# Kernel optimization log

Hardware: AMD Instinct MI355X
Metric: run time of the kernel (lower is better)

The kernel has to match this reference:

```python
import jax, jax.numpy as jnp
import numpy as np

CLASS_COUNT = 21
THRESHOLD = 0.5
ALPHA = 0.25
GAMMA = 2.0
VARIANCE = (0.1, 0.2)

B, A, N_OBJ = 32, 24576, 16


def point_form(boxes):
    # center form (cx, cy, w, h) -> point form (xmin, ymin, xmax, ymax)
    return jnp.concatenate([boxes[:, :2] - boxes[:, 2:] / 2,
                            boxes[:, :2] + boxes[:, 2:] / 2], axis=1)


def jaccard(truths, priors):
    # truths [N,4], priors [A,4] both in point form -> IoU [N, A]
    lt = jnp.maximum(truths[:, None, :2], priors[None, :, :2])
    rb = jnp.minimum(truths[:, None, 2:], priors[None, :, 2:])
    wh = jnp.clip(rb - lt, 0.0, None)
    inter = wh[..., 0] * wh[..., 1]
    area_t = ((truths[:, 2] - truths[:, 0]) * (truths[:, 3] - truths[:, 1]))[:, None]
    area_p = ((priors[:, 2] - priors[:, 0]) * (priors[:, 3] - priors[:, 1]))[None, :]
    return inter / (area_t + area_p - inter)


def match_one(labels, truths, anchors):
    # labels [N] int, truths [N,4] point form, anchors [A,4] center form
    overlaps = jaccard(truths, point_form(anchors))           # [N, A]
    best_prior_idx = jnp.argmax(overlaps, axis=1)             # [N]
    best_truth_overlap = jnp.max(overlaps, axis=0)            # [A]
    best_truth_idx = jnp.argmax(overlaps, axis=0)             # [A]
    # ensure every gt matches its best prior
    best_truth_overlap = best_truth_overlap.at[best_prior_idx].set(2.0)
    best_truth_idx = best_truth_idx.at[best_prior_idx].set(jnp.arange(truths.shape[0]))
    matches = truths[best_truth_idx]                          # [A, 4]
    conf = jnp.where(best_truth_overlap < THRESHOLD, 0, labels[best_truth_idx])
    # encode with variances
    g_cxcy = ((matches[:, :2] + matches[:, 2:]) * 0.5 - anchors[:, :2]) / (VARIANCE[0] * anchors[:, 2:])
    g_wh = jnp.log((matches[:, 2:] - matches[:, :2]) / anchors[:, 2:]) / VARIANCE[1]
    return conf, jnp.concatenate([g_cxcy, g_wh], axis=1)


def setup_inputs() -> dict:
    key = jax.random.key(0)
    k1, k2, k3, k4, k5, k6, k7 = jax.random.split(key, 7)
    class_preds = jax.random.normal(k1, (B, A, CLASS_COUNT), dtype=jnp.float32)
    loc_preds = jax.random.normal(k2, (B, A, 4), dtype=jnp.float32)
    # ground-truth boxes: random valid point-form boxes in [0,1]
    ctr = jax.random.uniform(k3, (B, N_OBJ, 2), minval=0.2, maxval=0.8)
    wh = jax.random.uniform(k4, (B, N_OBJ, 2), minval=0.05, maxval=0.3)
    loc_targets = jnp.clip(jnp.concatenate([ctr - wh / 2, ctr + wh / 2], axis=-1), 0.0, 1.0)
    class_targets = jax.random.randint(k5, (B, N_OBJ), 1, CLASS_COUNT)
    # anchors in center form
    a_ctr = jax.random.uniform(k6, (A, 2), minval=0.05, maxval=0.95)
    a_wh = jax.random.uniform(k7, (A, 2), minval=0.05, maxval=0.4)
    anchors = jnp.concatenate([a_ctr, a_wh], axis=1)
    return {"class_preds": class_preds, "loc_preds": loc_preds,
            "loc_targets": loc_targets, "anchors": anchors,
            "class_targets": class_targets}


def reference(class_preds, loc_preds, loc_targets, anchors, class_targets):
    conf, loc_t = jax.vmap(match_one, in_axes=(0, 0, None))(class_targets, loc_targets, anchors)
    pos = conf > 0                                            # [B, A]
    num_matched = jnp.sum(pos).astype(jnp.float32)
    # smooth L1 over positive anchors (sum reduction, beta=1)
    d = loc_preds - loc_t
    ad = jnp.abs(d)
    sl1 = jnp.where(ad < 1.0, 0.5 * d * d, ad - 0.5)
    loc_loss = jnp.sum(sl1 * pos[..., None].astype(sl1.dtype))
    # focal loss (drop background column 0)
    cp = class_preds.reshape(-1, CLASS_COUNT)[:, 1:]          # [B*A, C-1]
    t = jax.nn.one_hot(conf.reshape(-1), CLASS_COUNT, dtype=cp.dtype)[:, 1:]
    p = jax.nn.sigmoid(cp)
    pt = jnp.where(t > 0, p, 1.0 - p)
    w = (1.0 - pt) ** GAMMA
    w = jnp.where(t > 0, ALPHA * w, (1.0 - ALPHA) * w)
    # stable binary cross entropy with logits, weighted, sum reduction
    bce = jnp.maximum(cp, 0.0) - cp * t + jnp.log1p(jnp.exp(-jnp.abs(cp)))
    class_loss = jnp.sum(w * bce)
    class_loss = class_loss / num_matched
    loc_loss = loc_loss / num_matched
    return jnp.stack([class_loss, loc_loss, class_loss + loc_loss])
```

## Files before the change

kernel.cpp:

```cpp
#include <hip/hip_runtime.h>

#define A_COUNT 24576
#define B_COUNT 32
#define NOBJ 16
#define C_COUNT 21

#define NM 48
#define CHUNK (A_COUNT / NM)
#define NBLK_M (NM * B_COUNT)
#define NBLK_F 2048
#define GRID (NBLK_F + NBLK_M)
#define TOTAL4 (B_COUNT * A_COUNT * C_COUNT / 4)
#define STRIDE4F (NBLK_F * 256)

#define WS_BPP 0
#define WS_LOCP 196608
#define WS_CORP 202752
#define WS_POSP 208896
#define WS_CLSP 215040
#define WS_DLOC 223232
#define WS_DCLS 223360
#define WS_DPOS 223488

__device__ __forceinline__ unsigned long long pack_key(float iou, int a) {
    unsigned int ib = __float_as_uint(iou);
    return ((unsigned long long)ib << 32) | (unsigned long long)(0xFFFFFFFFu - (unsigned int)a);
}

__device__ __forceinline__ float iou_pf(float tx0, float ty0, float tx1, float ty1, float at,
                                        float x0, float y0, float x1, float y1, float ap) {
    float lx = fmaxf(tx0, x0), ly = fmaxf(ty0, y0);
    float rx = fminf(tx1, x1), ry = fminf(ty1, y1);
    float w = fmaxf(rx - lx, 0.0f), h = fmaxf(ry - ly, 0.0f);
    float inter = w * h;
    return inter * __builtin_amdgcn_rcpf(at + ap - inter);
}

__device__ __forceinline__ float sl1(float d) {
    float ad = fabsf(d);
    return (ad < 1.0f) ? 0.5f * d * d : ad - 0.5f;
}

__device__ __forceinline__ float loc_term(float4 t, float4 an, float4 lp) {
    float gx = ((t.x + t.z) * 0.5f - an.x) / (0.1f * an.z);
    float gy = ((t.y + t.w) * 0.5f - an.y) / (0.1f * an.w);
    float gw = __logf((t.z - t.x) / an.z) * 5.0f;
    float gh = __logf((t.w - t.y) / an.w) * 5.0f;
    return sl1(lp.x - gx) + sl1(lp.y - gy) + sl1(lp.z - gw) + sl1(lp.w - gh);
}

__device__ __forceinline__ float corr_term(float x) {
    float E = __expf(x);
    float den = 1.0f + E;
    float s = __builtin_amdgcn_rcpf(den);
    float p = E * s;
    float L = __logf(den);
    return 0.25f * s * s * (L - x) - 0.75f * p * p * L;
}

#define FOC(xval, rr, acc) {                                 \
    float E_ = __expf(xval);                                 \
    float den_ = 1.0f + E_;                                  \
    float s_ = __builtin_amdgcn_rcpf(den_);                  \
    float p_ = E_ * s_;                                      \
    float L_ = __logf(den_);                                 \
    float v_ = ((rr) == 0 || (rr) == 21) ? 0.0f : p_ * p_ * L_; \
    acc += v_; }

__global__ __launch_bounds__(256, 8) void k_phase1(const float* __restrict__ cls,
                                                   const float4* __restrict__ locp,
                                                   const float4* __restrict__ anchors,
                                                   const float4* __restrict__ truths,
                                                   const int* __restrict__ labels,
                                                   unsigned long long* __restrict__ bp_partial,
                                                   float* __restrict__ loc_partial,
                                                   float* __restrict__ corr_partial,
                                                   unsigned int* __restrict__ pos_partial,
                                                   float* __restrict__ cls_partial) {
    const int bid = blockIdx.x;
    const int tid = threadIdx.x;
    const int wv = tid >> 6, ln = tid & 63;
    __shared__ float s_red[4];

    if (bid < NBLK_F) {
        const float4* cls4 = (const float4*)cls;
        float acc0 = 0.0f, acc1 = 0.0f, acc2 = 0.0f, acc3 = 0.0f;
        int i = bid * 256 + tid;
        unsigned int f = (unsigned int)i * 4u;
        unsigned int dq = f / 21u;
        int r = (int)(f - dq * 21u);
        for (; i < TOTAL4; i += STRIDE4F) {
            float4 x4 = cls4[i];
            FOC(x4.x, r + 0, acc0); FOC(x4.y, r + 1, acc1);
            FOC(x4.z, r + 2, acc2); FOC(x4.w, r + 3, acc3);
            r += 8; if (r >= 21) r -= 21;
        }
        float cls_acc = 0.75f * ((acc0 + acc1) + (acc2 + acc3));
#pragma unroll
        for (int s = 32; s >= 1; s >>= 1) cls_acc += __shfl_xor(cls_acc, s);
        if (ln == 0) s_red[wv] = cls_acc;
        __syncthreads();
        if (tid == 0) cls_partial[bid] = s_red[0] + s_red[1] + s_red[2] + s_red[3];
        return;
    }

    const int mb = bid - NBLK_F;
    const int ch = mb % NM;
    const int b = mb / NM;
    __shared__ float4 s_t[NOBJ];
    __shared__ float s_area[NOBJ];
    __shared__ int s_lab[NOBJ];
    __shared__ unsigned long long s_w[NOBJ][4];
    if (tid < NOBJ) {
        float4 t = truths[b * NOBJ + tid];
        s_t[tid] = t;
        s_area[tid] = (t.z - t.x) * (t.w - t.y);
        s_lab[tid] = labels[b * NOBJ + tid];
    }
    __syncthreads();
    const int a0 = ch * CHUNK + tid;
    const int a1 = a0 + 256;
    float4 an0 = anchors[a0];
    float4 an1 = anchors[a1];
    float p0x0 = an0.x - an0.z * 0.5f, p0y0 = an0.y - an0.w * 0.5f;
    float p0x1 = an0.x + an0.z * 0.5f, p0y1 = an0.y + an0.w * 0.5f;
    float ap0 = (p0x1 - p0x0) * (p0y1 - p0y0);
    float p1x0 = an1.x - an1.z * 0.5f, p1y0 = an1.y - an1.w * 0.5f;
    float p1x1 = an1.x + an1.z * 0.5f, p1y1 = an1.y + an1.w * 0.5f;
    float ap1 = (p1x1 - p1x0) * (p1y1 - p1y0);
    float best0 = -1.0f, best1 = -1.0f;
    int idx0 = 0, idx1 = 0;
#pragma unroll
    for (int n = 0; n < NOBJ; ++n) {
        float4 t = s_t[n];
        float at = s_area[n];
        float iou0 = iou_pf(t.x, t.y, t.z, t.w, at, p0x0, p0y0, p0x1, p0y1, ap0);
        float iou1 = iou_pf(t.x, t.y, t.z, t.w, at, p1x0, p1y0, p1x1, p1y1, ap1);
        if (iou0 > best0) { best0 = iou0; idx0 = n; }
        if (iou1 > best1) { best1 = iou1; idx1 = n; }
        float lm = fmaxf(iou0, iou1);
        float m = lm;
#pragma unroll
        for (int s = 32; s >= 1; s >>= 1) m = fmaxf(m, __shfl_xor(m, s));
        unsigned long long mask = __ballot(lm == m);
        if (ln == __builtin_ctzll(mask)) {
            s_w[n][wv] = (iou0 == m) ? pack_key(iou0, a0) : pack_key(iou1, a1);
        }
    }
    __syncthreads();
    if (tid < NOBJ) {
        unsigned long long k = s_w[tid][0];
#pragma unroll
        for (int i = 1; i < 4; ++i) k = (s_w[tid][i] > k) ? s_w[tid][i] : k;
        bp_partial[(b * NOBJ + tid) * NM + ch] = k;
    }
    float loc_l = 0.0f, corr_acc = 0.0f;
    unsigned int pos = 0;
    if (!(best0 < 0.5f)) {
        pos++;
        loc_l += loc_term(s_t[idx0], an0, locp[(size_t)b * A_COUNT + a0]);
        corr_acc += corr_term(cls[((size_t)b * A_COUNT + a0) * C_COUNT + s_lab[idx0]]);
    }
    if (!(best1 < 0.5f)) {
        pos++;
        loc_l += loc_term(s_t[idx1], an1, locp[(size_t)b * A_COUNT + a1]);
        corr_acc += corr_term(cls[((size_t)b * A_COUNT + a1) * C_COUNT + s_lab[idx1]]);
    }
#pragma unroll
    for (int s = 32; s >= 1; s >>= 1) {
        loc_l += __shfl_xor(loc_l, s);
        corr_acc += __shfl_xor(corr_acc, s);
        pos += __shfl_xor(pos, s);
    }
    __shared__ float s_cr[4];
    __shared__ unsigned int s_pp[4];
    if (ln == 0) {
        s_red[wv] = loc_l;
        s_cr[wv] = corr_acc;
        s_pp[wv] = pos;
    }
    __syncthreads();
    if (tid == 0) {
        loc_partial[mb] = s_red[0] + s_red[1] + s_red[2] + s_red[3];
        corr_partial[mb] = s_cr[0] + s_cr[1] + s_cr[2] + s_cr[3];
        pos_partial[mb] = s_pp[0] + s_pp[1] + s_pp[2] + s_pp[3];
    }
}

__global__ __launch_bounds__(256) void k_fix(const float* __restrict__ cls,
                                             const float4* __restrict__ locp,
                                             const float4* __restrict__ anchors,
                                             const float4* __restrict__ truths,
                                             const int* __restrict__ labels,
                                             const unsigned long long* __restrict__ bp_partial,
                                             float* __restrict__ dloc,
                                             float* __restrict__ dcls,
                                             int* __restrict__ dpos) {
    const int b = blockIdx.x;
    const int tid = threadIdx.x;
    __shared__ int s_bp[NOBJ];
    {
        const int g = tid >> 4, l = tid & 15;
        const unsigned long long* pp = &bp_partial[(size_t)(b * NOBJ + g) * NM];
        unsigned long long k = pp[l];
#pragma unroll
        for (int kk = 1; kk < 3; ++kk) {
            unsigned long long v = pp[l + 16 * kk];
            k = (v > k) ? v : k;
        }
#pragma unroll
        for (int s = 8; s >= 1; s >>= 1) {
            unsigned long long o = __shfl_xor(k, s);
            k = (o > k) ? o : k;
        }
        if (l == 0) {
            unsigned int ia = 0xFFFFFFFFu - (unsigned int)(k & 0xFFFFFFFFull);
            s_bp[g] = (ia >= A_COUNT) ? -1 : (int)ia;
        }
    }
    __syncthreads();
    float d_loc = 0.0f, d_cls = 0.0f;
    int d_pos = 0;
    if (tid < NOBJ) {
        const int n = tid;
        const int q = s_bp[n];
        bool winner = (q >= 0);
        for (int n2 = n + 1; n2 < NOBJ; ++n2)
            if (s_bp[n2] == q) winner = false;
        if (winner) {
            float4 an = anchors[q];
            float px0 = an.x - an.z * 0.5f, py0 = an.y - an.w * 0.5f;
            float px1 = an.x + an.z * 0.5f, py1 = an.y + an.w * 0.5f;
            float ap = (px1 - px0) * (py1 - py0);
            float best = -1.0f;
            int idx = 0;
            for (int n2 = 0; n2 < NOBJ; ++n2) {
                float4 t = truths[b * NOBJ + n2];
                float at = (t.z - t.x) * (t.w - t.y);
                float iou = iou_pf(t.x, t.y, t.z, t.w, at, px0, py0, px1, py1, ap);
                if (iou > best) { best = iou; idx = n2; }
            }
            float4 lp = locp[(size_t)b * A_COUNT + q];
            if (!(best < 0.5f)) {
                d_pos -= 1;
                d_loc -= loc_term(truths[b * NOBJ + idx], an, lp);
                d_cls -= corr_term(cls[((size_t)b * A_COUNT + q) * C_COUNT + labels[b * NOBJ + idx]]);
            }
            d_pos += 1;
            d_loc += loc_term(truths[b * NOBJ + n], an, lp);
            d_cls += corr_term(cls[((size_t)b * A_COUNT + q) * C_COUNT + labels[b * NOBJ + n]]);
        }
    }
    if (tid < 64) {
#pragma unroll
        for (int s = 8; s >= 1; s >>= 1) {
            d_loc += __shfl_xor(d_loc, s);
            d_cls += __shfl_xor(d_cls, s);
            d_pos += __shfl_xor(d_pos, s);
        }
        if (tid == 0) {
            dloc[b] = d_loc;
            dcls[b] = d_cls;
            dpos[b] = d_pos;
        }
    }
}

__global__ __launch_bounds__(256) void k_final(const float* __restrict__ loc_partial,
                                               const float* __restrict__ corr_partial,
                                               const unsigned int* __restrict__ pos_partial,
                                               const float* __restrict__ cls_partial,
                                               const float* __restrict__ dloc,
                                               const float* __restrict__ dcls,
                                               const int* __restrict__ dpos,
                                               float* __restrict__ out) {
    const int tid = threadIdx.x;
    double loc = 0.0, clsv = 0.0;
    int pos = 0;
    for (int i = tid; i < NBLK_M; i += 256) {
        loc += (double)loc_partial[i];
        clsv += (double)corr_partial[i];
        pos += (int)pos_partial[i];
    }
    for (int i = tid; i < NBLK_F; i += 256) clsv += (double)cls_partial[i];
    if (tid < B_COUNT) {
        loc += (double)dloc[tid];
        clsv += (double)dcls[tid];
        pos += dpos[tid];
    }
#pragma unroll
    for (int s = 32; s >= 1; s >>= 1) {
        loc += __shfl_xor(loc, s);
        clsv += __shfl_xor(clsv, s);
        pos += __shfl_xor(pos, s);
    }
    __shared__ double s_l[4], s_c[4];
    __shared__ int s_p[4];
    if ((tid & 63) == 0) {
        s_l[tid >> 6] = loc;
        s_c[tid >> 6] = clsv;
        s_p[tid >> 6] = pos;
    }
    __syncthreads();
    if (tid == 0) {
        double L = s_l[0] + s_l[1] + s_l[2] + s_l[3];
        double Cv = s_c[0] + s_c[1] + s_c[2] + s_c[3];
        float nm = (float)(s_p[0] + s_p[1] + s_p[2] + s_p[3]);
        float cf = (float)Cv / nm;
        float lf = (float)L / nm;
        out[0] = cf;
        out[1] = lf;
        out[2] = cf + lf;
    }
}

extern "C" void kernel_launch(void* const* d_in, const int* in_sizes, int n_in,
                              void* d_out, int out_size, void* d_ws, size_t ws_size,
                              hipStream_t stream) {
    const float* cls = (const float*)d_in[0];
    const float4* locp = (const float4*)d_in[1];
    const float4* truths = (const float4*)d_in[2];
    const float4* anchors = (const float4*)d_in[3];
    const int* labels = (const int*)d_in[4];

    char* ws = (char*)d_ws;
    unsigned long long* bp_partial = (unsigned long long*)(ws + WS_BPP);
    float* loc_partial = (float*)(ws + WS_LOCP);
    float* corr_partial = (float*)(ws + WS_CORP);
    unsigned int* pos_partial = (unsigned int*)(ws + WS_POSP);
    float* cls_partial = (float*)(ws + WS_CLSP);
    float* dloc = (float*)(ws + WS_DLOC);
    float* dcls = (float*)(ws + WS_DCLS);
    int* dpos = (int*)(ws + WS_DPOS);

    k_phase1<<<GRID, 256, 0, stream>>>(cls, locp, anchors, truths, labels, bp_partial,
                                       loc_partial, corr_partial, pos_partial, cls_partial);
    k_fix<<<B_COUNT, 256, 0, stream>>>(cls, locp, anchors, truths, labels, bp_partial,
                                       dloc, dcls, dpos);
    k_final<<<1, 256, 0, stream>>>(loc_partial, corr_partial, pos_partial, cls_partial,
                                   dloc, dcls, dpos, (float*)d_out);
}
```

Baseline: 46.15 us.

## Split fused phase-1 kernel into separate focal and match kernels with prefetch

Splits the heterogeneous phase-1 kernel, which branched on block index between focal-loss streaming and anchor matching, into two dedicated kernels launched one after the other on the same stream. The focal kernel also gains a software-prefetch loop that loads the next float4 before computing the current one, to hide memory latency. Each kernel can now be compiled with its own register budget instead of one shared budget. The cost is one extra launch, and the match blocks can no longer run concurrently with the focal blocks.

```diff
diff --git a/kernel.cpp b/kernel.cpp
--- a/kernel.cpp
+++ b/kernel.cpp
@@ -9,7 +9,6 @@
 #define CHUNK (A_COUNT / NM)
 #define NBLK_M (NM * B_COUNT)
 #define NBLK_F 2048
-#define GRID (NBLK_F + NBLK_M)
 #define TOTAL4 (B_COUNT * A_COUNT * C_COUNT / 4)
 #define STRIDE4F (NBLK_F * 256)
 
@@ -67,46 +66,51 @@
     float v_ = ((rr) == 0 || (rr) == 21) ? 0.0f : p_ * p_ * L_; \
     acc += v_; }
 
-__global__ __launch_bounds__(256, 8) void k_phase1(const float* __restrict__ cls,
-                                                   const float4* __restrict__ locp,
-                                                   const float4* __restrict__ anchors,
-                                                   const float4* __restrict__ truths,
-                                                   const int* __restrict__ labels,
-                                                   unsigned long long* __restrict__ bp_partial,
-                                                   float* __restrict__ loc_partial,
-                                                   float* __restrict__ corr_partial,
-                                                   unsigned int* __restrict__ pos_partial,
-                                                   float* __restrict__ cls_partial) {
-    const int bid = blockIdx.x;
+__global__ __launch_bounds__(256) void k_focal(const float4* __restrict__ cls4,
+                                               float* __restrict__ cls_partial) {
     const int tid = threadIdx.x;
     const int wv = tid >> 6, ln = tid & 63;
+    int i = blockIdx.x * 256 + tid;
+    unsigned int f = (unsigned int)i * 4u;
+    unsigned int dq = f / 21u;
+    int r = (int)(f - dq * 21u);
+    float acc0 = 0.0f, acc1 = 0.0f, acc2 = 0.0f, acc3 = 0.0f;
+    float4 cur = cls4[i];
+    for (;;) {
+        const int inext = i + STRIDE4F;
+        const bool more = inext < TOTAL4;
+        float4 nxt;
+        if (more) nxt = cls4[inext];
+        FOC(cur.x, r + 0, acc0); FOC(cur.y, r + 1, acc1);
+        FOC(cur.z, r + 2, acc2); FOC(cur.w, r + 3, acc3);
+        if (!more) break;
+        cur = nxt;
+        i = inext;
+        r += 8; if (r >= 21) r -= 21;
+    }
+    float cls_acc = 0.75f * ((acc0 + acc1) + (acc2 + acc3));
+#pragma unroll
+    for (int s = 32; s >= 1; s >>= 1) cls_acc += __shfl_xor(cls_acc, s);
     __shared__ float s_red[4];
-
-    if (bid < NBLK_F) {
-        const float4* cls4 = (const float4*)cls;
-        float acc0 = 0.0f, acc1 = 0.0f, acc2 = 0.0f, acc3 = 0.0f;
-        int i = bid * 256 + tid;
-        unsigned int f = (unsigned int)i * 4u;
-        unsigned int dq = f / 21u;
-        int r = (int)(f - dq * 21u);
-        for (; i < TOTAL4; i += STRIDE4F) {
-            float4 x4 = cls4[i];
-            FOC(x4.x, r + 0, acc0); FOC(x4.y, r + 1, acc1);
-            FOC(x4.z, r + 2, acc2); FOC(x4.w, r + 3, acc3);
-            r += 8; if (r >= 21) r -= 21;
-        }
-        float cls_acc = 0.75f * ((acc0 + acc1) + (acc2 + acc3));
-#pragma unroll
-        for (int s = 32; s >= 1; s >>= 1) cls_acc += __shfl_xor(cls_acc, s);
-        if (ln == 0) s_red[wv] = cls_acc;
-        __syncthreads();
-        if (tid == 0) cls_partial[bid] = s_red[0] + s_red[1] + s_red[2] + s_red[3];
-        return;
-    }
-
-    const int mb = bid - NBLK_F;
+    if (ln == 0) s_red[wv] = cls_acc;
+    __syncthreads();
+    if (tid == 0) cls_partial[blockIdx.x] = s_red[0] + s_red[1] + s_red[2] + s_red[3];
+}
+
+__global__ __launch_bounds__(256) void k_match(const float* __restrict__ cls,
+                                               const float4* __restrict__ locp,
+                                               const float4* __restrict__ anchors,
+                                               const float4* __restrict__ truths,
+                                               const int* __restrict__ labels,
+                                               unsigned long long* __restrict__ bp_partial,
+                                               float* __restrict__ loc_partial,
+                                               float* __restrict__ corr_partial,
+                                               unsigned int* __restrict__ pos_partial) {
+    const int mb = blockIdx.x;
     const int ch = mb % NM;
     const int b = mb / NM;
+    const int tid = threadIdx.x;
+    const int wv = tid >> 6, ln = tid & 63;
     __shared__ float4 s_t[NOBJ];
     __shared__ float s_area[NOBJ];
     __shared__ int s_lab[NOBJ];
@@ -172,16 +176,16 @@
         corr_acc += __shfl_xor(corr_acc, s);
         pos += __shfl_xor(pos, s);
     }
-    __shared__ float s_cr[4];
+    __shared__ float s_ll[4], s_cr[4];
     __shared__ unsigned int s_pp[4];
     if (ln == 0) {
-        s_red[wv] = loc_l;
+        s_ll[wv] = loc_l;
         s_cr[wv] = corr_acc;
         s_pp[wv] = pos;
     }
     __syncthreads();
     if (tid == 0) {
-        loc_partial[mb] = s_red[0] + s_red[1] + s_red[2] + s_red[3];
+        loc_partial[mb] = s_ll[0] + s_ll[1] + s_ll[2] + s_ll[3];
         corr_partial[mb] = s_cr[0] + s_cr[1] + s_cr[2] + s_cr[3];
         pos_partial[mb] = s_pp[0] + s_pp[1] + s_pp[2] + s_pp[3];
     }
@@ -333,8 +337,9 @@
     float* dcls = (float*)(ws + WS_DCLS);
     int* dpos = (int*)(ws + WS_DPOS);
 
-    k_phase1<<<GRID, 256, 0, stream>>>(cls, locp, anchors, truths, labels, bp_partial,
-                                       loc_partial, corr_partial, pos_partial, cls_partial);
+    k_focal<<<NBLK_F, 256, 0, stream>>>((const float4*)cls, cls_partial);
+    k_match<<<NBLK_M, 256, 0, stream>>>(cls, locp, anchors, truths, labels, bp_partial,
+                                        loc_partial, corr_partial, pos_partial);
     k_fix<<<B_COUNT, 256, 0, stream>>>(cls, locp, anchors, truths, labels, bp_partial,
                                        dloc, dcls, dpos);
     k_final<<<1, 256, 0, stream>>>(loc_partial, corr_partial, pos_partial, cls_partial,
```

New measurement: 45.93 us. Within noise of the previous version (-0.5%).
